# Optimization experiments

Measured on AMD Instinct MI355X. Metric: run time of the kernel, lower is better.

Reference implementation:

```python
import jax, jax.numpy as jnp
import numpy as np

NUM_LEVELS = 16
FEATS_PER_LEVEL = 2
LOG2_HASHMAP = 19
TABLE_SIZE = 1 << LOG2_HASHMAP
BASE_RES = 16
DESIRED_RES = 4096
PER_LEVEL_SCALE = float(np.exp(np.log(DESIRED_RES / BASE_RES) / (NUM_LEVELS - 1)))
PRIMES = (np.uint32(1), np.uint32(2654435761), np.uint32(805459861))
N_POINTS = 2_000_000


def _level_features(x, table, level):
    # x: [N,3] in [0,1]; table: [TABLE_SIZE, F]
    scale = BASE_RES * (PER_LEVEL_SCALE ** level) - 1.0
    res = int(np.ceil(scale)) + 1
    dense = (res ** 3) <= TABLE_SIZE  # tcnn uses dense indexing when grid fits
    pos = x * scale + 0.5
    pos0 = jnp.floor(pos)
    w = pos - pos0                     # trilinear weights, [N,3]
    base = pos0.astype(jnp.uint32)
    out = jnp.zeros((x.shape[0], table.shape[1]), dtype=table.dtype)
    for c in range(8):                 # 8 corners of the voxel
        offs = [(c >> d) & 1 for d in range(3)]
        pc = [jnp.minimum(base[:, d] + np.uint32(offs[d]), np.uint32(res - 1)) for d in range(3)]
        if dense:
            idx = pc[0] + pc[1] * np.uint32(res) + pc[2] * np.uint32(res * res)
        else:
            idx = (pc[0] * PRIMES[0]) ^ (pc[1] * PRIMES[1]) ^ (pc[2] * PRIMES[2])
            idx = idx & np.uint32(TABLE_SIZE - 1)
        wt = jnp.ones(x.shape[0], dtype=x.dtype)
        for d in range(3):
            wt = wt * (w[:, d] if offs[d] else (1.0 - w[:, d]))
        out = out + wt[:, None] * table[idx.astype(jnp.int32)]
    return out


def hashgrid_encode(x, tables):
    # x: [N,3] in [0,1]; tables: [L, TABLE_SIZE, F] -> [N, L*F]
    return jnp.concatenate(
        [_level_features(x, tables[l], l) for l in range(NUM_LEVELS)], axis=-1)


def setup_inputs() -> dict:
    key = jax.random.key(0)
    k1, k2, k3, k4, k5 = jax.random.split(key, 5)
    points = jax.random.uniform(k1, (N_POINTS, 3), dtype=jnp.float32)
    # tcnn hashgrid init: uniform(-1e-4, 1e-4)
    tables = jax.random.uniform(k2, (NUM_LEVELS, TABLE_SIZE, FEATS_PER_LEVEL),
                                minval=-1e-4, maxval=1e-4, dtype=jnp.float32)
    def kaiming(k, fan_out, fan_in):
        bound = np.sqrt(2.0) * np.sqrt(3.0 / fan_in)
        return jax.random.uniform(k, (fan_out, fan_in), minval=-bound, maxval=bound,
                                  dtype=jnp.float32)
    W1 = kaiming(k3, 32, 32)
    W2 = kaiming(k4, 32, 32)
    W3 = kaiming(k5, 4, 32)
    aabb = jnp.stack([jnp.zeros(3, jnp.float32), jnp.ones(3, jnp.float32)])
    return {"points": points, "tables": tables, "W1": W1, "W2": W2, "W3": W3,
            "aabb": aabb}


def reference(points, tables, W1, W2, W3, aabb):
    texc = jnp.clip((points - aabb[0][None, :]) / (aabb[1] - aabb[0])[None, :], 0.0, 1.0)
    enc = hashgrid_encode(texc, tables)            # [N, 32]
    h = jax.nn.relu(enc @ W1.T)
    h = jax.nn.relu(h @ W2.T)
    out = h @ W3.T                                 # [N, 4]
    mn = jnp.array([0.0, 0.0, 0.0, 0.01], dtype=out.dtype)
    mx = jnp.array([1.0, 1.0, 1.0, 1.0], dtype=out.dtype)
    return jax.nn.sigmoid(out) * (mx - mn) + mn
```

## Files before the change

kernel.cpp:

```cpp
#include <hip/hip_runtime.h>
#include <cmath>


namespace {
constexpr int kLevels = 16;
constexpr unsigned kTableSize = 1u << 19;
constexpr unsigned kMask = kTableSize - 1u;

typedef _Float16 half2_t __attribute__((ext_vector_type(2)));
typedef unsigned int u32;

struct LevelParams {
  float scale[kLevels];
  unsigned res[kLevels];
  int dense[kLevels];
};
}

__global__ __launch_bounds__(256)
void conv_tables_kernel(const float2* __restrict__ src, half2_t* __restrict__ dst,
                        int n_entries,
                        const float* __restrict__ W1, const float* __restrict__ W2,
                        const float* __restrict__ W3, half2_t* __restrict__ Wh)
{
  int i = blockIdx.x * blockDim.x + threadIdx.x;
  if (i < 512) {
    Wh[i] = half2_t{(_Float16)W1[2 * i], (_Float16)W1[2 * i + 1]};
  } else if (i < 1024) {
    int t = i - 512;
    Wh[512 + t] = half2_t{(_Float16)W2[2 * t], (_Float16)W2[2 * t + 1]};
  } else if (i < 1088) {
    int t = i - 1024;
    Wh[1024 + t] = half2_t{(_Float16)W3[2 * t], (_Float16)W3[2 * t + 1]};
  }
  int stride = gridDim.x * blockDim.x;
  for (; i < n_entries; i += stride) {
    float2 v = src[i];
    dst[i] = half2_t{(_Float16)v.x, (_Float16)v.y};
  }
}

__device__ __forceinline__ u32 sel4(uint4 v, u32 j) {
  u32 lo = (j & 1u) ? v.y : v.x;
  u32 hi = (j & 1u) ? v.w : v.z;
  return (j & 2u) ? hi : lo;
}

__global__ __launch_bounds__(256)
void encode_kernel(const float* __restrict__ points,
                   const u32* __restrict__ tables,
                   const float* __restrict__ aabb,
                   half2_t* __restrict__ enc,
                   LevelParams lp, int n, int bpl)
{
  int l = blockIdx.x / bpl;
  int i = (blockIdx.x - l * bpl) * blockDim.x + threadIdx.x;
  if (i >= n) return;

  float a0x = aabb[0], a0y = aabb[1], a0z = aabb[2];
  float a1x = aabb[3], a1y = aabb[4], a1z = aabb[5];
  float x = fminf(fmaxf((points[3 * i + 0] - a0x) / (a1x - a0x), 0.f), 1.f);
  float y = fminf(fmaxf((points[3 * i + 1] - a0y) / (a1y - a0y), 0.f), 1.f);
  float z = fminf(fmaxf((points[3 * i + 2] - a0z) / (a1z - a0z), 0.f), 1.f);

  float s = lp.scale[l];
  unsigned res = lp.res[l];
  bool dense = (lp.dense[l] != 0);
  unsigned rm1 = res - 1u;
  unsigned res2 = res * res;
  const u32* tab = tables + (size_t)l * kTableSize;

  float fx = x * s + 0.5f, fy = y * s + 0.5f, fz = z * s + 0.5f;
  float fx0 = floorf(fx), fy0 = floorf(fy), fz0 = floorf(fz);
  float wx = fx - fx0, wy = fy - fy0, wz = fz - fz0;
  unsigned bx = (unsigned)fx0, by = (unsigned)fy0, bz = (unsigned)fz0;

  unsigned pcx0 = min(bx, rm1), pcx1 = min(bx + 1u, rm1);

  u32 idx0[4], idx1[4];
  #pragma unroll
  for (int p = 0; p < 4; ++p) {
    unsigned oy = (unsigned)(p & 1);
    unsigned oz = (unsigned)(p >> 1);
    unsigned pcy = min(by + oy, rm1);
    unsigned pcz = min(bz + oz, rm1);
    if (dense) {
      u32 b = pcy * res + pcz * res2;
      idx0[p] = pcx0 + b;
      idx1[p] = pcx1 + b;
    } else {
      u32 h = (pcy * 2654435761u) ^ (pcz * 805459861u);
      idx0[p] = (pcx0 ^ h) & kMask;
      idx1[p] = (pcx1 ^ h) & kMask;
    }
  }

  uint4 v[4];
  #pragma unroll
  for (int p = 0; p < 4; ++p)
    v[p] = *reinterpret_cast<const uint4*>(tab + (idx0[p] & ~3u));

  u32 e1x[4] = {0u, 0u, 0u, 0u};
  #pragma unroll
  for (int p = 0; p < 4; ++p) {
    if ((idx0[p] ^ idx1[p]) >= 4u) e1x[p] = tab[idx1[p]];
  }

  float wx1 = wx, wx0 = 1.f - wx;
  float acc0 = 0.f, acc1 = 0.f;
  #pragma unroll
  for (int p = 0; p < 4; ++p) {
    unsigned oy = (unsigned)(p & 1);
    unsigned oz = (unsigned)(p >> 1);
    float wyz = (oy ? wy : 1.f - wy) * (oz ? wz : 1.f - wz);
    u32 e0 = sel4(v[p], idx0[p] & 3u);
    u32 e1g = sel4(v[p], idx1[p] & 3u);
    u32 e1 = ((idx0[p] ^ idx1[p]) < 4u) ? e1g : e1x[p];
    half2_t f0 = __builtin_bit_cast(half2_t, e0);
    half2_t f1 = __builtin_bit_cast(half2_t, e1);
    float w0 = wyz * wx0, w1 = wyz * wx1;
    acc0 += w0 * (float)f0.x + w1 * (float)f1.x;
    acc1 += w0 * (float)f0.y + w1 * (float)f1.y;
  }
  enc[(size_t)l * n + i] = half2_t{(_Float16)acc0, (_Float16)acc1};
}

__device__ __forceinline__ float dot2_acc(half2_t a, half2_t b, float c) {
#if __has_builtin(__builtin_amdgcn_fdot2)
  return __builtin_amdgcn_fdot2(a, b, c, false);
#else
  return c + (float)a.x * (float)b.x + (float)a.y * (float)b.y;
#endif
}

__global__ __launch_bounds__(256)
void mlp_kernel(const half2_t* __restrict__ enc,
                const half2_t* __restrict__ Wh,
                float* __restrict__ out, int n)
{
  int i = blockIdx.x * blockDim.x + threadIdx.x;
  if (i >= n) return;

  half2_t e[16];
  #pragma unroll
  for (int l = 0; l < kLevels; ++l) e[l] = enc[(size_t)l * n + i];

  const half2_t* W1h = Wh;
  const half2_t* W2h = Wh + 512;
  const half2_t* W3h = Wh + 1024;

  float h1f[32];
  #pragma unroll
  for (int j = 0; j < 32; ++j) {
    float acc = 0.f;
    #pragma unroll
    for (int k = 0; k < 16; ++k) acc = dot2_acc(e[k], W1h[16 * j + k], acc);
    h1f[j] = fmaxf(acc, 0.f);
  }
  half2_t h1[16];
  #pragma unroll
  for (int k = 0; k < 16; ++k)
    h1[k] = half2_t{(_Float16)h1f[2 * k], (_Float16)h1f[2 * k + 1]};

  float h2f[32];
  #pragma unroll
  for (int j = 0; j < 32; ++j) {
    float acc = 0.f;
    #pragma unroll
    for (int k = 0; k < 16; ++k) acc = dot2_acc(h1[k], W2h[16 * j + k], acc);
    h2f[j] = fmaxf(acc, 0.f);
  }
  half2_t h2[16];
  #pragma unroll
  for (int k = 0; k < 16; ++k)
    h2[k] = half2_t{(_Float16)h2f[2 * k], (_Float16)h2f[2 * k + 1]};

  float o[4];
  #pragma unroll
  for (int j = 0; j < 4; ++j) {
    float acc = 0.f;
    #pragma unroll
    for (int k = 0; k < 16; ++k) acc = dot2_acc(h2[k], W3h[16 * j + k], acc);
    o[j] = acc;
  }

  float4 r;
  r.x = 1.f / (1.f + __expf(-o[0]));
  r.y = 1.f / (1.f + __expf(-o[1]));
  r.z = 1.f / (1.f + __expf(-o[2]));
  r.w = 0.99f / (1.f + __expf(-o[3])) + 0.01f;
  reinterpret_cast<float4*>(out)[i] = r;
}

__global__ __launch_bounds__(256)
void hashgrid_mlp_kernel(const float* __restrict__ points,
                         const float* __restrict__ tables,
                         const float* __restrict__ W1,
                         const float* __restrict__ W2,
                         const float* __restrict__ W3,
                         const float* __restrict__ aabb,
                         float* __restrict__ out,
                         LevelParams lp, int n)
{
  int i = blockIdx.x * blockDim.x + threadIdx.x;
  if (i >= n) return;
  float a0x = aabb[0], a0y = aabb[1], a0z = aabb[2];
  float a1x = aabb[3], a1y = aabb[4], a1z = aabb[5];
  float x = fminf(fmaxf((points[3 * i + 0] - a0x) / (a1x - a0x), 0.f), 1.f);
  float y = fminf(fmaxf((points[3 * i + 1] - a0y) / (a1y - a0y), 0.f), 1.f);
  float z = fminf(fmaxf((points[3 * i + 2] - a0z) / (a1z - a0z), 0.f), 1.f);
  float enc[2 * kLevels];
  #pragma unroll
  for (int l = 0; l < kLevels; ++l) {
    float s = lp.scale[l];
    unsigned res = lp.res[l];
    bool dense = (lp.dense[l] != 0);
    unsigned rm1 = res - 1u;
    unsigned res2 = res * res;
    float fx = x * s + 0.5f, fy = y * s + 0.5f, fz = z * s + 0.5f;
    float fx0 = floorf(fx), fy0 = floorf(fy), fz0 = floorf(fz);
    float wx = fx - fx0, wy = fy - fy0, wz = fz - fz0;
    unsigned bx = (unsigned)fx0, by = (unsigned)fy0, bz = (unsigned)fz0;
    const float2* tab = reinterpret_cast<const float2*>(tables) + (size_t)l * kTableSize;
    float acc0 = 0.f, acc1 = 0.f;
    #pragma unroll
    for (int c = 0; c < 8; ++c) {
      unsigned ox = (unsigned)(c & 1);
      unsigned oy = (unsigned)((c >> 1) & 1);
      unsigned oz = (unsigned)((c >> 2) & 1);
      unsigned pcx = min(bx + ox, rm1);
      unsigned pcy = min(by + oy, rm1);
      unsigned pcz = min(bz + oz, rm1);
      unsigned idx;
      if (dense) idx = pcx + pcy * res + pcz * res2;
      else idx = (pcx ^ (pcy * 2654435761u) ^ (pcz * 805459861u)) & kMask;
      float wt = (ox ? wx : 1.f - wx) * (oy ? wy : 1.f - wy) * (oz ? wz : 1.f - wz);
      float2 f = tab[idx];
      acc0 += wt * f.x;
      acc1 += wt * f.y;
    }
    enc[2 * l + 0] = acc0;
    enc[2 * l + 1] = acc1;
  }
  float h1[32];
  #pragma unroll
  for (int j = 0; j < 32; ++j) {
    float acc = 0.f;
    #pragma unroll
    for (int k = 0; k < 32; ++k) acc += enc[k] * W1[32 * j + k];
    h1[j] = fmaxf(acc, 0.f);
  }
  float h2[32];
  #pragma unroll
  for (int j = 0; j < 32; ++j) {
    float acc = 0.f;
    #pragma unroll
    for (int k = 0; k < 32; ++k) acc += h1[k] * W2[32 * j + k];
    h2[j] = fmaxf(acc, 0.f);
  }
  float o[4];
  #pragma unroll
  for (int j = 0; j < 4; ++j) {
    float acc = 0.f;
    #pragma unroll
    for (int k = 0; k < 32; ++k) acc += h2[k] * W3[32 * j + k];
    o[j] = acc;
  }
  float4 r;
  r.x = 1.f / (1.f + __expf(-o[0]));
  r.y = 1.f / (1.f + __expf(-o[1]));
  r.z = 1.f / (1.f + __expf(-o[2]));
  r.w = 0.99f / (1.f + __expf(-o[3])) + 0.01f;
  reinterpret_cast<float4*>(out)[i] = r;
}

extern "C" void kernel_launch(void* const* d_in, const int* in_sizes, int n_in,
                              void* d_out, int out_size, void* d_ws, size_t ws_size,
                              hipStream_t stream) {
  const float* points = (const float*)d_in[0];
  const float* tables = (const float*)d_in[1];
  const float* W1     = (const float*)d_in[2];
  const float* W2     = (const float*)d_in[3];
  const float* W3     = (const float*)d_in[4];
  const float* aabb   = (const float*)d_in[5];
  float* out = (float*)d_out;
  int n = in_sizes[0] / 3;

  LevelParams lp;
  const double pls = std::exp(std::log(4096.0 / 16.0) / 15.0);
  for (int l = 0; l < kLevels; ++l) {
    double s = 16.0 * std::pow(pls, (double)l) - 1.0;
    lp.scale[l] = (float)s;
    long long res = (long long)std::ceil(s) + 1;
    lp.res[l] = (unsigned)res;
    lp.dense[l] = (res * res * res <= (long long)kTableSize) ? 1 : 0;
  }

  const int block = 256;
  const size_t tab_f16_bytes = (size_t)kLevels * kTableSize * sizeof(half2_t);
  const size_t enc_bytes     = (size_t)kLevels * (size_t)n * sizeof(half2_t);
  const size_t w_bytes       = 1088 * sizeof(half2_t);
  const size_t needed = tab_f16_bytes + enc_bytes + w_bytes;

  if (ws_size >= needed) {
    half2_t* tab_f16 = reinterpret_cast<half2_t*>(d_ws);
    half2_t* enc = reinterpret_cast<half2_t*>((char*)d_ws + tab_f16_bytes);
    half2_t* Wh  = reinterpret_cast<half2_t*>((char*)d_ws + tab_f16_bytes + enc_bytes);

    const int n_entries = kLevels * (int)kTableSize;
    conv_tables_kernel<<<2048, block, 0, stream>>>(
        reinterpret_cast<const float2*>(tables), tab_f16, n_entries, W1, W2, W3, Wh);

    const int bpl = (n + block - 1) / block;
    encode_kernel<<<bpl * kLevels, block, 0, stream>>>(
        points, reinterpret_cast<const u32*>(tab_f16), aabb, enc, lp, n, bpl);

    mlp_kernel<<<(n + block - 1) / block, block, 0, stream>>>(enc, Wh, out, n);
  } else {
    const int grid = (n + block - 1) / block;
    hashgrid_mlp_kernel<<<grid, block, 0, stream>>>(
        points, tables, W1, W2, W3, aabb, out, lp, n);
  }
}
```

Before: 768.8 us.

## Spatially sort points by Morton cell before hash-grid encoding

Adds a counting sort of points into 64^3 Morton-ordered cells (histogram, three-pass scan, atomic scatter), so the encode kernel processes spatially coherent points and table lookups hit cache better. The MLP writes results back through a permutation array. This adds several extra kernels, global atomics and a scattered output write, and needs a larger workspace. It falls back to the previous unsorted path when the workspace is too small.

```diff
diff --git a/kernel.cpp b/kernel.cpp
--- a/kernel.cpp
+++ b/kernel.cpp
@@ -6,6 +6,8 @@
 constexpr int kLevels = 16;
 constexpr unsigned kTableSize = 1u << 19;
 constexpr unsigned kMask = kTableSize - 1u;
+constexpr int kNumCells = 1 << 18;
+constexpr int kScanBlocks = kNumCells / 256;
 
 typedef _Float16 half2_t __attribute__((ext_vector_type(2)));
 typedef unsigned int u32;
@@ -15,6 +17,22 @@
   unsigned res[kLevels];
   int dense[kLevels];
 };
+}
+
+__device__ __forceinline__ u32 part1by2(u32 x) {
+  x &= 0x3FFu;
+  x = (x | (x << 16)) & 0x030000FFu;
+  x = (x | (x << 8))  & 0x0300F00Fu;
+  x = (x | (x << 4))  & 0x030C30C3u;
+  x = (x | (x << 2))  & 0x09249249u;
+  return x;
+}
+
+__device__ __forceinline__ u32 cell_of(float x, float y, float z) {
+  u32 cx = min((u32)(x * 64.f), 63u);
+  u32 cy = min((u32)(y * 64.f), 63u);
+  u32 cz = min((u32)(z * 64.f), 63u);
+  return part1by2(cx) | (part1by2(cy) << 1) | (part1by2(cz) << 2);
 }
 
 __global__ __launch_bounds__(256)
@@ -40,28 +58,102 @@
   }
 }
 
-__device__ __forceinline__ u32 sel4(uint4 v, u32 j) {
-  u32 lo = (j & 1u) ? v.y : v.x;
-  u32 hi = (j & 1u) ? v.w : v.z;
-  return (j & 2u) ? hi : lo;
-}
-
-__global__ __launch_bounds__(256)
-void encode_kernel(const float* __restrict__ points,
-                   const u32* __restrict__ tables,
-                   const float* __restrict__ aabb,
-                   half2_t* __restrict__ enc,
-                   LevelParams lp, int n, int bpl)
-{
-  int l = blockIdx.x / bpl;
-  int i = (blockIdx.x - l * bpl) * blockDim.x + threadIdx.x;
+__global__ __launch_bounds__(256)
+void hist_kernel(const float* __restrict__ points, const float* __restrict__ aabb,
+                 u32* __restrict__ hist, int n)
+{
+  int i = blockIdx.x * blockDim.x + threadIdx.x;
   if (i >= n) return;
-
   float a0x = aabb[0], a0y = aabb[1], a0z = aabb[2];
   float a1x = aabb[3], a1y = aabb[4], a1z = aabb[5];
   float x = fminf(fmaxf((points[3 * i + 0] - a0x) / (a1x - a0x), 0.f), 1.f);
   float y = fminf(fmaxf((points[3 * i + 1] - a0y) / (a1y - a0y), 0.f), 1.f);
   float z = fminf(fmaxf((points[3 * i + 2] - a0z) / (a1z - a0z), 0.f), 1.f);
+  atomicAdd(&hist[cell_of(x, y, z)], 1u);
+}
+
+__global__ __launch_bounds__(256)
+void scan1_kernel(u32* __restrict__ hist, u32* __restrict__ totals)
+{
+  __shared__ u32 s[256];
+  int t = threadIdx.x;
+  int base = blockIdx.x * 256;
+  u32 v = hist[base + t];
+  s[t] = v;
+  __syncthreads();
+  #pragma unroll
+  for (int off = 1; off < 256; off <<= 1) {
+    u32 a = (t >= off) ? s[t - off] : 0u;
+    __syncthreads();
+    s[t] += a;
+    __syncthreads();
+  }
+  if (t == 255) totals[blockIdx.x] = s[255];
+  hist[base + t] = s[t] - v;
+}
+
+__global__ __launch_bounds__(1024)
+void scan2_kernel(u32* __restrict__ totals)
+{
+  __shared__ u32 s[kScanBlocks];
+  int t = threadIdx.x;
+  u32 v = totals[t];
+  s[t] = v;
+  __syncthreads();
+  #pragma unroll
+  for (int off = 1; off < kScanBlocks; off <<= 1) {
+    u32 a = (t >= off) ? s[t - off] : 0u;
+    __syncthreads();
+    s[t] += a;
+    __syncthreads();
+  }
+  totals[t] = s[t] - v;
+}
+
+__global__ __launch_bounds__(256)
+void scan3_kernel(u32* __restrict__ hist, const u32* __restrict__ totals)
+{
+  int t = threadIdx.x;
+  int base = blockIdx.x * 256;
+  hist[base + t] += totals[blockIdx.x];
+}
+
+__global__ __launch_bounds__(256)
+void scatter_kernel(const float* __restrict__ points, const float* __restrict__ aabb,
+                    u32* __restrict__ offs,
+                    float* __restrict__ sx, float* __restrict__ sy,
+                    float* __restrict__ sz, u32* __restrict__ perm, int n)
+{
+  int i = blockIdx.x * blockDim.x + threadIdx.x;
+  if (i >= n) return;
+  float a0x = aabb[0], a0y = aabb[1], a0z = aabb[2];
+  float a1x = aabb[3], a1y = aabb[4], a1z = aabb[5];
+  float x = fminf(fmaxf((points[3 * i + 0] - a0x) / (a1x - a0x), 0.f), 1.f);
+  float y = fminf(fmaxf((points[3 * i + 1] - a0y) / (a1y - a0y), 0.f), 1.f);
+  float z = fminf(fmaxf((points[3 * i + 2] - a0z) / (a1z - a0z), 0.f), 1.f);
+  u32 pos = atomicAdd(&offs[cell_of(x, y, z)], 1u);
+  sx[pos] = x; sy[pos] = y; sz[pos] = z;
+  perm[pos] = (u32)i;
+}
+
+__device__ __forceinline__ u32 sel4(uint4 v, u32 j) {
+  u32 lo = (j & 1u) ? v.y : v.x;
+  u32 hi = (j & 1u) ? v.w : v.z;
+  return (j & 2u) ? hi : lo;
+}
+
+__global__ __launch_bounds__(256)
+void encode_sorted_kernel(const float* __restrict__ sx, const float* __restrict__ sy,
+                          const float* __restrict__ sz,
+                          const u32* __restrict__ tables,
+                          half2_t* __restrict__ enc,
+                          LevelParams lp, int n, int bpl)
+{
+  int l = blockIdx.x / bpl;
+  int i = (blockIdx.x - l * bpl) * blockDim.x + threadIdx.x;
+  if (i >= n) return;
+
+  float x = sx[i], y = sy[i], z = sz[i];
 
   float s = lp.scale[l];
   unsigned res = lp.res[l];
@@ -136,6 +228,7 @@
 __global__ __launch_bounds__(256)
 void mlp_kernel(const half2_t* __restrict__ enc,
                 const half2_t* __restrict__ Wh,
+                const u32* __restrict__ perm,
                 float* __restrict__ out, int n)
 {
   int i = blockIdx.x * blockDim.x + threadIdx.x;
@@ -189,7 +282,83 @@
   r.y = 1.f / (1.f + __expf(-o[1]));
   r.z = 1.f / (1.f + __expf(-o[2]));
   r.w = 0.99f / (1.f + __expf(-o[3])) + 0.01f;
-  reinterpret_cast<float4*>(out)[i] = r;
+  int oi = perm ? (int)perm[i] : i;
+  reinterpret_cast<float4*>(out)[oi] = r;
+}
+
+__global__ __launch_bounds__(256)
+void encode_raw_kernel(const float* __restrict__ points,
+                       const u32* __restrict__ tables,
+                       const float* __restrict__ aabb,
+                       half2_t* __restrict__ enc,
+                       LevelParams lp, int n, int bpl)
+{
+  int l = blockIdx.x / bpl;
+  int i = (blockIdx.x - l * bpl) * blockDim.x + threadIdx.x;
+  if (i >= n) return;
+
+  float a0x = aabb[0], a0y = aabb[1], a0z = aabb[2];
+  float a1x = aabb[3], a1y = aabb[4], a1z = aabb[5];
+  float x = fminf(fmaxf((points[3 * i + 0] - a0x) / (a1x - a0x), 0.f), 1.f);
+  float y = fminf(fmaxf((points[3 * i + 1] - a0y) / (a1y - a0y), 0.f), 1.f);
+  float z = fminf(fmaxf((points[3 * i + 2] - a0z) / (a1z - a0z), 0.f), 1.f);
+
+  float s = lp.scale[l];
+  unsigned res = lp.res[l];
+  bool dense = (lp.dense[l] != 0);
+  unsigned rm1 = res - 1u;
+  unsigned res2 = res * res;
+  const u32* tab = tables + (size_t)l * kTableSize;
+
+  float fx = x * s + 0.5f, fy = y * s + 0.5f, fz = z * s + 0.5f;
+  float fx0 = floorf(fx), fy0 = floorf(fy), fz0 = floorf(fz);
+  float wx = fx - fx0, wy = fy - fy0, wz = fz - fz0;
+  unsigned bx = (unsigned)fx0, by = (unsigned)fy0, bz = (unsigned)fz0;
+  unsigned pcx0 = min(bx, rm1), pcx1 = min(bx + 1u, rm1);
+
+  u32 idx0[4], idx1[4];
+  #pragma unroll
+  for (int p = 0; p < 4; ++p) {
+    unsigned oy = (unsigned)(p & 1);
+    unsigned oz = (unsigned)(p >> 1);
+    unsigned pcy = min(by + oy, rm1);
+    unsigned pcz = min(bz + oz, rm1);
+    if (dense) {
+      u32 b = pcy * res + pcz * res2;
+      idx0[p] = pcx0 + b;
+      idx1[p] = pcx1 + b;
+    } else {
+      u32 h = (pcy * 2654435761u) ^ (pcz * 805459861u);
+      idx0[p] = (pcx0 ^ h) & kMask;
+      idx1[p] = (pcx1 ^ h) & kMask;
+    }
+  }
+  uint4 v[4];
+  #pragma unroll
+  for (int p = 0; p < 4; ++p)
+    v[p] = *reinterpret_cast<const uint4*>(tab + (idx0[p] & ~3u));
+  u32 e1x[4] = {0u, 0u, 0u, 0u};
+  #pragma unroll
+  for (int p = 0; p < 4; ++p) {
+    if ((idx0[p] ^ idx1[p]) >= 4u) e1x[p] = tab[idx1[p]];
+  }
+  float wx1 = wx, wx0 = 1.f - wx;
+  float acc0 = 0.f, acc1 = 0.f;
+  #pragma unroll
+  for (int p = 0; p < 4; ++p) {
+    unsigned oy = (unsigned)(p & 1);
+    unsigned oz = (unsigned)(p >> 1);
+    float wyz = (oy ? wy : 1.f - wy) * (oz ? wz : 1.f - wz);
+    u32 e0 = sel4(v[p], idx0[p] & 3u);
+    u32 e1g = sel4(v[p], idx1[p] & 3u);
+    u32 e1 = ((idx0[p] ^ idx1[p]) < 4u) ? e1g : e1x[p];
+    half2_t f0 = __builtin_bit_cast(half2_t, e0);
+    half2_t f1 = __builtin_bit_cast(half2_t, e1);
+    float w0 = wyz * wx0, w1 = wyz * wx1;
+    acc0 += w0 * (float)f0.x + w1 * (float)f1.x;
+    acc1 += w0 * (float)f0.y + w1 * (float)f1.y;
+  }
+  enc[(size_t)l * n + i] = half2_t{(_Float16)acc0, (_Float16)acc1};
 }
 
 __global__ __launch_bounds__(256)
@@ -297,28 +466,60 @@
   }
 
   const int block = 256;
-  const size_t tab_f16_bytes = (size_t)kLevels * kTableSize * sizeof(half2_t);
-  const size_t enc_bytes     = (size_t)kLevels * (size_t)n * sizeof(half2_t);
-  const size_t w_bytes       = 1088 * sizeof(half2_t);
-  const size_t needed = tab_f16_bytes + enc_bytes + w_bytes;
-
-  if (ws_size >= needed) {
-    half2_t* tab_f16 = reinterpret_cast<half2_t*>(d_ws);
-    half2_t* enc = reinterpret_cast<half2_t*>((char*)d_ws + tab_f16_bytes);
-    half2_t* Wh  = reinterpret_cast<half2_t*>((char*)d_ws + tab_f16_bytes + enc_bytes);
-
-    const int n_entries = kLevels * (int)kTableSize;
+  const int n_entries = kLevels * (int)kTableSize;
+  const int grid_n = (n + block - 1) / block;
+
+  auto align256 = [](size_t v) { return (v + 255) & ~(size_t)255; };
+  const size_t tab_b   = align256((size_t)n_entries * 4);
+  const size_t enc_b   = align256((size_t)kLevels * n * 4);
+  const size_t wh_b    = align256(1088 * 4);
+  const size_t hist_b  = align256((size_t)kNumCells * 4);
+  const size_t tot_b   = align256((size_t)kScanBlocks * 4);
+  const size_t sxyz_b  = align256((size_t)n * 4);
+  const size_t perm_b  = align256((size_t)n * 4);
+  const size_t need_sorted = tab_b + enc_b + wh_b + hist_b + tot_b + 3 * sxyz_b + perm_b;
+  const size_t need_r3     = tab_b + enc_b + wh_b;
+
+  if (ws_size >= need_sorted) {
+    char* p = (char*)d_ws;
+    half2_t* tab_f16 = (half2_t*)p;            p += tab_b;
+    half2_t* enc     = (half2_t*)p;            p += enc_b;
+    half2_t* Wh      = (half2_t*)p;            p += wh_b;
+    u32* hist        = (u32*)p;                p += hist_b;
+    u32* totals      = (u32*)p;                p += tot_b;
+    float* sx        = (float*)p;              p += sxyz_b;
+    float* sy        = (float*)p;              p += sxyz_b;
+    float* sz        = (float*)p;              p += sxyz_b;
+    u32* perm        = (u32*)p;
+
+    hipMemsetAsync(hist, 0, (size_t)kNumCells * 4, stream);
+
     conv_tables_kernel<<<2048, block, 0, stream>>>(
         reinterpret_cast<const float2*>(tables), tab_f16, n_entries, W1, W2, W3, Wh);
 
-    const int bpl = (n + block - 1) / block;
-    encode_kernel<<<bpl * kLevels, block, 0, stream>>>(
-        points, reinterpret_cast<const u32*>(tab_f16), aabb, enc, lp, n, bpl);
-
-    mlp_kernel<<<(n + block - 1) / block, block, 0, stream>>>(enc, Wh, out, n);
+    hist_kernel<<<grid_n, block, 0, stream>>>(points, aabb, hist, n);
+    scan1_kernel<<<kScanBlocks, 256, 0, stream>>>(hist, totals);
+    scan2_kernel<<<1, kScanBlocks, 0, stream>>>(totals);
+    scan3_kernel<<<kScanBlocks, 256, 0, stream>>>(hist, totals);
+    scatter_kernel<<<grid_n, block, 0, stream>>>(points, aabb, hist, sx, sy, sz, perm, n);
+
+    encode_sorted_kernel<<<grid_n * kLevels, block, 0, stream>>>(
+        sx, sy, sz, reinterpret_cast<const u32*>(tab_f16), enc, lp, n, grid_n);
+
+    mlp_kernel<<<grid_n, block, 0, stream>>>(enc, Wh, perm, out, n);
+  } else if (ws_size >= need_r3) {
+    char* p = (char*)d_ws;
+    half2_t* tab_f16 = (half2_t*)p;            p += tab_b;
+    half2_t* enc     = (half2_t*)p;            p += enc_b;
+    half2_t* Wh      = (half2_t*)p;
+
+    conv_tables_kernel<<<2048, block, 0, stream>>>(
+        reinterpret_cast<const float2*>(tables), tab_f16, n_entries, W1, W2, W3, Wh);
+    encode_raw_kernel<<<grid_n * kLevels, block, 0, stream>>>(
+        points, reinterpret_cast<const u32*>(tab_f16), aabb, enc, lp, n, grid_n);
+    mlp_kernel<<<grid_n, block, 0, stream>>>(enc, Wh, nullptr, out, n);
   } else {
-    const int grid = (n + block - 1) / block;
-    hashgrid_mlp_kernel<<<grid, block, 0, stream>>>(
+    hashgrid_mlp_kernel<<<grid_n, block, 0, stream>>>(
         points, tables, W1, W2, W3, aabb, out, lp, n);
   }
 }
```

After: 902.7 us. 17.4% more time.
